# Optimization experiments

Measured on AMD Instinct MI355X. Metric: run time of the kernel, lower is better.

The kernel has to match this reference:

```python
import jax, jax.numpy as jnp
import numpy as np

B, S, D, H, NL, FE = 2, 1024, 1024, 16, 6, 4
HD = D // H
DFF = D * FE
EPS = 1e-5


def setup_inputs() -> dict:
    key = jax.random.key(0)
    ks = jax.random.split(key, 12)
    sd = 0.02
    n = lambda k, sh: (jax.random.normal(k, sh, jnp.float32) * sd)
    return {
        "x": jax.random.normal(ks[0], (B, S, D), jnp.float32),
        "pos": n(ks[1], (1, S, D)),
        "Wq": n(ks[2], (NL, HD, HD)), "bq": jnp.zeros((NL, HD), jnp.float32),
        "Wk": n(ks[3], (NL, HD, HD)), "bk": jnp.zeros((NL, HD), jnp.float32),
        "Wv": n(ks[4], (NL, HD, HD)), "bv": jnp.zeros((NL, HD), jnp.float32),
        "Wfc": n(ks[5], (NL, D, D)), "bfc": jnp.zeros((NL, D), jnp.float32),
        "ln1_w": jnp.ones((NL, D), jnp.float32), "ln1_b": jnp.zeros((NL, D), jnp.float32),
        "ln2_w": jnp.ones((NL, D), jnp.float32), "ln2_b": jnp.zeros((NL, D), jnp.float32),
        "W1": n(ks[6], (NL, D, DFF)), "b1": jnp.zeros((NL, DFF), jnp.float32),
        "W2": n(ks[7], (NL, DFF, D)), "b2": jnp.zeros((NL, D), jnp.float32),
        "lnf_w": jnp.ones((D,), jnp.float32), "lnf_b": jnp.zeros((D,), jnp.float32),
    }


def _ln(z, w, b):
    m = jnp.mean(z, axis=-1, keepdims=True)
    v = jnp.mean(jnp.square(z - m), axis=-1, keepdims=True)
    return (z - m) * jax.lax.rsqrt(v + EPS) * w + b


def reference(x, pos, Wq, bq, Wk, bk, Wv, bv, Wfc, bfc,
              ln1_w, ln1_b, ln2_w, ln2_b, W1, b1, W2, b2, lnf_w, lnf_b):
    Bx, Sx, Dx = x.shape
    causal = jnp.tril(jnp.ones((Sx, Sx), bool))  # [S,S], broadcast over b,h
    y = x + pos[:, :Sx, :]
    scale = 1.0 / jnp.sqrt(jnp.float32(HD))
    for i in range(NL):
        yh = y.reshape(Bx, Sx, H, HD)
        # per-head Linear with weights SHARED across heads (as in source)
        q = yh @ Wq[i] + bq[i]
        k = yh @ Wk[i] + bk[i]
        v = yh @ Wv[i] + bv[i]
        score = jnp.einsum("bqhd,bkhd->bhqk", q, k)
        # masked_fill(-1e20) BEFORE scaling, as in source
        score = jnp.where(causal, score, jnp.float32(-1e20)) * scale
        attn = jax.nn.softmax(score, axis=-1)
        o = jnp.einsum("bhqk,bkhd->bqhd", attn, v).reshape(Bx, Sx, D)
        o = o @ Wfc[i] + bfc[i]
        add = _ln(o + y, ln1_w[i], ln1_b[i])
        ff = jax.nn.gelu(add @ W1[i] + b1[i], approximate=False) @ W2[i] + b2[i]
        y = _ln(ff + add, ln2_w[i], ln2_b[i])
    return _ln(y, lnf_w, lnf_b)
```

## Files before the change

kernel.cpp:

```cpp
#include <hip/hip_runtime.h>
#include <hip/hip_bf16.h>
#include <math.h>

#define B_   2
#define S_   1024
#define D_   1024
#define H_   16
#define HD_  64
#define NL_  6
#define DFF_ 4096

typedef __bf16 bf16_t;
typedef bf16_t bf16x8 __attribute__((ext_vector_type(8)));
typedef bf16_t bf16x4 __attribute__((ext_vector_type(4)));
typedef float  f32x4  __attribute__((ext_vector_type(4)));

__device__ __forceinline__ float gelu_exact(float x) {
    return 0.5f * x * (1.0f + erff(x * 0.70710678118654752f));
}

__device__ __forceinline__ void gload16(const bf16_t* g, bf16_t* l) {
    __builtin_amdgcn_global_load_lds(
        (const __attribute__((address_space(1))) void*)g,
        (__attribute__((address_space(3))) void*)l, 16, 0, 0);
}

__global__ __launch_bounds__(256) void add_pos_kernel(
    const float* __restrict__ x, const float* __restrict__ pos,
    float* __restrict__ y, bf16_t* __restrict__ yb)
{
    int idx = blockIdx.x * 256 + threadIdx.x;
    f32x4 xv = *(const f32x4*)&x[idx * 4];
    f32x4 pv = *(const f32x4*)&pos[(idx & 262143) * 4];
    f32x4 o = xv + pv;
    *(f32x4*)&y[idx * 4] = o;
    *(bf16x4*)&yb[idx * 4] = __builtin_convertvector(o, bf16x4);
}

__global__ __launch_bounds__(256) void qkv_mfma_kernel(
    const bf16_t* __restrict__ yb,
    const float* __restrict__ Wq, const float* __restrict__ bq,
    const float* __restrict__ Wk, const float* __restrict__ bk,
    const float* __restrict__ Wv, const float* __restrict__ bv,
    bf16_t* __restrict__ q, bf16_t* __restrict__ k, bf16_t* __restrict__ v)
{
    __shared__ __align__(16) bf16_t As[128][72];
    __shared__ __align__(16) bf16_t Wt[3][64][72];

    int tid = threadIdx.x;
    long m0 = (long)blockIdx.x * 128;

#pragma unroll
    for (int it = 0; it < 4; ++it) {
        int c = it * 256 + tid;
        int row = c >> 3, col = (c & 7) * 8;
        *(bf16x8*)&As[row][col] = *(const bf16x8*)&yb[(m0 + row) * 64 + col];
    }
#pragma unroll
    for (int it = 0; it < 16; ++it) {
        int i = it * 256 + tid;
        int r = i >> 6, c = i & 63;
        Wt[0][c][r] = (bf16_t)Wq[i];
        Wt[1][c][r] = (bf16_t)Wk[i];
        Wt[2][c][r] = (bf16_t)Wv[i];
    }
    __syncthreads();

    int wave = tid >> 6, lane = tid & 63;
    int quad = lane >> 4, l16 = lane & 15;
    int wm = wave * 32;

    bf16x8 a[2][2];
#pragma unroll
    for (int i = 0; i < 2; ++i)
#pragma unroll
        for (int ks = 0; ks < 2; ++ks)
            a[i][ks] = *(bf16x8*)&As[wm + i * 16 + l16][ks * 32 + quad * 8];

    f32x4 acc[3][2][4];
#pragma unroll
    for (int o = 0; o < 3; ++o)
#pragma unroll
        for (int i = 0; i < 2; ++i)
#pragma unroll
            for (int j = 0; j < 4; ++j) acc[o][i][j] = (f32x4)0.f;

#pragma unroll
    for (int o = 0; o < 3; ++o)
#pragma unroll
        for (int j = 0; j < 4; ++j) {
            bf16x8 b0 = *(bf16x8*)&Wt[o][j * 16 + l16][quad * 8];
            bf16x8 b1 = *(bf16x8*)&Wt[o][j * 16 + l16][32 + quad * 8];
#pragma unroll
            for (int i = 0; i < 2; ++i) {
                acc[o][i][j] = __builtin_amdgcn_mfma_f32_16x16x32_bf16(a[i][0], b0, acc[o][i][j], 0, 0, 0);
                acc[o][i][j] = __builtin_amdgcn_mfma_f32_16x16x32_bf16(a[i][1], b1, acc[o][i][j], 0, 0, 0);
            }
        }

    bf16_t* outs[3] = { q, k, v };
    const float* biases[3] = { bq, bk, bv };
#pragma unroll
    for (int o = 0; o < 3; ++o)
#pragma unroll
        for (int j = 0; j < 4; ++j) {
            int col = j * 16 + l16;
            float bias = biases[o][col];
#pragma unroll
            for (int i = 0; i < 2; ++i) {
                long rbase = m0 + wm + i * 16 + quad * 4;
#pragma unroll
                for (int r = 0; r < 4; ++r)
                    outs[o][(rbase + r) * 64 + col] = (bf16_t)(acc[o][i][j][r] + bias);
            }
        }
}

__global__ __launch_bounds__(256) void vtrans_kernel(
    const bf16_t* __restrict__ vb, bf16_t* __restrict__ vT)
{
    __shared__ __align__(16) bf16_t L[32][72];
    int tid = threadIdx.x;
    int s0 = blockIdx.x * 32;
    int bh = blockIdx.y;
    int b = bh >> 4, h = bh & 15;
    int sr = tid >> 3, dc = (tid & 7) * 8;
    *(bf16x8*)&L[sr][dc] =
        *(const bf16x8*)&vb[(((long)b * S_ + s0 + sr) * H_ + h) * HD_ + dc];
    __syncthreads();
    int dr = tid >> 2, sg = (tid & 3) * 8;
    bf16x8 o;
#pragma unroll
    for (int j = 0; j < 8; ++j) o[j] = L[sg + j][dr];
    *(bf16x8*)&vT[((long)bh * HD_ + dr) * S_ + s0 + sg] = o;
}

__global__ __launch_bounds__(256) void attn_mfma_kernel(
    const bf16_t* __restrict__ Q, const bf16_t* __restrict__ K,
    const bf16_t* __restrict__ VT, bf16_t* __restrict__ Ob)
{
    __shared__ __align__(16) bf16_t Ks[32][72];
    __shared__ __align__(16) bf16_t Vt[64][40];
    __shared__ __align__(16) bf16_t Ps[4][16][40];

    int tid = threadIdx.x;
    int wave = tid >> 6, lane = tid & 63;
    int quad = lane >> 4, l16 = lane & 15;
    int q0 = blockIdx.x * 64;
    int bh = blockIdx.y;
    int b = bh >> 4, h = bh & 15;
    int qw = q0 + wave * 16;
    const float scale = 0.125f;
    const float MASKED = -1.25e19f;

    const bf16_t* Qbase = Q + (((long)b * S_ + qw + l16) * H_ + h) * HD_;
    bf16x8 aq0 = *(const bf16x8*)&Qbase[quad * 8];
    bf16x8 aq1 = *(const bf16x8*)&Qbase[32 + quad * 8];

    float mrun = -3.0e38f, lrun = 0.f;
    f32x4 oacc[4];
#pragma unroll
    for (int n = 0; n < 4; ++n) oacc[n] = (f32x4)0.f;

    int srow = tid >> 3, scol = (tid & 7) * 8;
    int vdr = tid >> 2, vkg = (tid & 3) * 8;
    const bf16_t* VTbase = VT + ((long)bh * HD_ + vdr) * S_ + vkg;
    int qg = qw + l16;

    int nkt = (q0 + 64) / 32;
    for (int kt = 0; kt < nkt; ++kt) {
        int k0 = kt * 32;
        __syncthreads();
        *(bf16x8*)&Ks[srow][scol] =
            *(const bf16x8*)&K[(((long)b * S_ + k0 + srow) * H_ + h) * HD_ + scol];
        *(bf16x8*)&Vt[vdr][vkg] = *(const bf16x8*)&VTbase[k0];
        __syncthreads();

        if (k0 > qw + 15) continue;

        f32x4 sc[2];
        sc[0] = (f32x4)0.f; sc[1] = (f32x4)0.f;
#pragma unroll
        for (int n = 0; n < 2; ++n) {
            bf16x8 ak0 = *(bf16x8*)&Ks[n * 16 + l16][quad * 8];
            bf16x8 ak1 = *(bf16x8*)&Ks[n * 16 + l16][32 + quad * 8];
            sc[n] = __builtin_amdgcn_mfma_f32_16x16x32_bf16(ak0, aq0, sc[n], 0, 0, 0);
            sc[n] = __builtin_amdgcn_mfma_f32_16x16x32_bf16(ak1, aq1, sc[n], 0, 0, 0);
        }
        float pmax = MASKED;
#pragma unroll
        for (int n = 0; n < 2; ++n)
#pragma unroll
            for (int r = 0; r < 4; ++r) {
                int kv = k0 + n * 16 + quad * 4 + r;
                float sv = (kv <= qg) ? sc[n][r] * scale : MASKED;
                sc[n][r] = sv;
                pmax = fmaxf(pmax, sv);
            }
        pmax = fmaxf(pmax, __shfl_xor(pmax, 16));
        pmax = fmaxf(pmax, __shfl_xor(pmax, 32));
        float mnew = fmaxf(mrun, pmax);
        float ls = 0.f;
#pragma unroll
        for (int n = 0; n < 2; ++n)
#pragma unroll
            for (int r = 0; r < 4; ++r) {
                float pv = __expf(sc[n][r] - mnew);
                sc[n][r] = pv;
                ls += pv;
            }
        ls += __shfl_xor(ls, 16);
        ls += __shfl_xor(ls, 32);
        float alpha = __expf(mrun - mnew);
        lrun = lrun * alpha + ls;
        mrun = mnew;

        *(bf16x4*)&Ps[wave][l16][quad * 4]      = __builtin_convertvector(sc[0], bf16x4);
        *(bf16x4*)&Ps[wave][l16][16 + quad * 4] = __builtin_convertvector(sc[1], bf16x4);

        f32x4 av;
#pragma unroll
        for (int r = 0; r < 4; ++r) av[r] = __shfl(alpha, quad * 4 + r);

        bf16x8 pa = *(bf16x8*)&Ps[wave][l16][quad * 8];
#pragma unroll
        for (int n = 0; n < 4; ++n) {
            bf16x8 bv = *(bf16x8*)&Vt[n * 16 + l16][quad * 8];
            oacc[n] = __builtin_amdgcn_mfma_f32_16x16x32_bf16(pa, bv, oacc[n] * av, 0, 0, 0);
        }
    }

    float inv = 1.0f / lrun;
    f32x4 iv;
#pragma unroll
    for (int r = 0; r < 4; ++r) iv[r] = __shfl(inv, quad * 4 + r);
#pragma unroll
    for (int r = 0; r < 4; ++r) {
        long rowbase = (((long)b * S_ + qw + quad * 4 + r) * H_ + h) * HD_;
#pragma unroll
        for (int n = 0; n < 4; ++n)
            Ob[rowbase + n * 16 + l16] = (bf16_t)(oacc[n][r] * iv[r]);
    }
}

__global__ void tconv_kernel(const float* __restrict__ W, bf16_t* __restrict__ Wt,
                             int Kd, int Nd)
{
    __shared__ float t[32][33];
    int tx = threadIdx.x, ty = threadIdx.y;
    int bx = blockIdx.x, by = blockIdx.y;
#pragma unroll
    for (int i = 0; i < 4; ++i)
        t[ty + i * 8][tx] = W[(size_t)(by * 32 + ty + i * 8) * Nd + bx * 32 + tx];
    __syncthreads();
#pragma unroll
    for (int i = 0; i < 4; ++i)
        Wt[(size_t)(bx * 32 + ty + i * 8) * Kd + by * 32 + tx] = (bf16_t)t[tx][ty + i * 8];
}

__global__ __launch_bounds__(256) void gemm_bt_kernel(
    const bf16_t* __restrict__ A, const bf16_t* __restrict__ Bt,
    const float* __restrict__ bias, float* __restrict__ Cf,
    bf16_t* __restrict__ Cb, int M, int N, int K, int act, size_t pstride)
{
    __shared__ __align__(16) bf16_t As[128 * 32];
    __shared__ __align__(16) bf16_t Bs[64 * 32];
    int tid = threadIdx.x;
    int wave = tid >> 6, lane = tid & 63;
    int quad = lane >> 4, l16 = lane & 15;
    int m0 = blockIdx.x * 128;
    int n0 = blockIdx.y * 64;
    int Kc = K / gridDim.z;
    int kbeg = blockIdx.z * Kc;
    int kend = kbeg + Kc;
    float* Cfp = Cf ? Cf + (size_t)blockIdx.z * pstride : nullptr;

    int wm = (wave >> 1) * 64, wn = (wave & 1) * 32;

    int srow = lane >> 2;
    int sslot = (lane & 3) ^ (srow & 3);
    int rslot = (quad ^ (l16 & 3)) * 8;

    f32x4 acc[4][2];
#pragma unroll
    for (int i = 0; i < 4; ++i)
#pragma unroll
        for (int j = 0; j < 2; ++j) acc[i][j] = (f32x4)0.f;

    const bf16_t* Ab = A + (size_t)(m0 + srow) * K + sslot * 8;
    const bf16_t* Bb = Bt + (size_t)(n0 + wave * 16 + srow) * K + sslot * 8;

    for (int k0 = kbeg; k0 < kend; k0 += 32) {
        __syncthreads();
#pragma unroll
        for (int t = 0; t < 2; ++t) {
            int seg = wave * 2 + t;
            gload16(Ab + (size_t)seg * 16 * K + k0, &As[seg * 512]);
        }
        gload16(Bb + k0, &Bs[wave * 512]);
        __syncthreads();

        bf16x8 af[4], bfr[2];
#pragma unroll
        for (int i = 0; i < 4; ++i)
            af[i] = *(bf16x8*)&As[(wm + i * 16 + l16) * 32 + rslot];
#pragma unroll
        for (int j = 0; j < 2; ++j)
            bfr[j] = *(bf16x8*)&Bs[(wn + j * 16 + l16) * 32 + rslot];
#pragma unroll
        for (int i = 0; i < 4; ++i)
#pragma unroll
            for (int j = 0; j < 2; ++j)
                acc[i][j] = __builtin_amdgcn_mfma_f32_16x16x32_bf16(
                    af[i], bfr[j], acc[i][j], 0, 0, 0);
    }

#pragma unroll
    for (int j = 0; j < 2; ++j) {
        int col = n0 + wn + j * 16 + l16;
        float bv = (bias && blockIdx.z == 0) ? bias[col] : 0.f;
#pragma unroll
        for (int i = 0; i < 4; ++i) {
            int rbase = m0 + wm + i * 16 + quad * 4;
#pragma unroll
            for (int r = 0; r < 4; ++r) {
                float vv = acc[i][j][r] + bv;
                if (act == 1) vv = gelu_exact(vv);
                if (Cfp) Cfp[(size_t)(rbase + r) * N + col] = vv;
                if (Cb) Cb[(size_t)(rbase + r) * N + col] = (bf16_t)vv;
            }
        }
    }
}

__global__ __launch_bounds__(256) void ln_fused_kernel(
    const float* __restrict__ a0, const float* __restrict__ a1,
    const float* __restrict__ b,
    const float* __restrict__ w, const float* __restrict__ beta,
    float* __restrict__ out, bf16_t* __restrict__ outb)
{
    long row = blockIdx.x;
    int tid = threadIdx.x;
    f32x4 z = *(const f32x4*)&a0[row * D_ + tid * 4];
    if (a1) z += *(const f32x4*)&a1[row * D_ + tid * 4];
    if (b)  z += *(const f32x4*)&b[row * D_ + tid * 4];
    float s  = z[0] + z[1] + z[2] + z[3];
    float ss = z[0]*z[0] + z[1]*z[1] + z[2]*z[2] + z[3]*z[3];
#pragma unroll
    for (int off = 32; off >= 1; off >>= 1) {
        s  += __shfl_down(s, off);
        ss += __shfl_down(ss, off);
    }
    __shared__ float red[8];
    int lane = tid & 63, wid = tid >> 6;
    if (lane == 0) { red[wid * 2] = s; red[wid * 2 + 1] = ss; }
    __syncthreads();
    s  = red[0] + red[2] + red[4] + red[6];
    ss = red[1] + red[3] + red[5] + red[7];
    float mean = s * (1.0f / D_);
    float var  = ss * (1.0f / D_) - mean * mean;
    float rs = rsqrtf(var + 1e-5f);
    f32x4 wv = *(const f32x4*)&w[tid * 4];
    f32x4 bv = *(const f32x4*)&beta[tid * 4];
    f32x4 o = (z - mean) * rs * wv + bv;
    *(f32x4*)&out[row * D_ + tid * 4] = o;
    if (outb) *(bf16x4*)&outb[row * D_ + tid * 4] = __builtin_convertvector(o, bf16x4);
}

extern "C" void kernel_launch(void* const* d_in, const int* in_sizes, int n_in,
                              void* d_out, int out_size, void* d_ws, size_t ws_size,
                              hipStream_t stream)
{
    (void)in_sizes; (void)n_in; (void)out_size; (void)ws_size;
    const float* x    = (const float*)d_in[0];
    const float* pos  = (const float*)d_in[1];
    const float* Wq   = (const float*)d_in[2];
    const float* bq   = (const float*)d_in[3];
    const float* Wk   = (const float*)d_in[4];
    const float* bk   = (const float*)d_in[5];
    const float* Wv   = (const float*)d_in[6];
    const float* bv   = (const float*)d_in[7];
    const float* Wfc  = (const float*)d_in[8];
    const float* bfc  = (const float*)d_in[9];
    const float* ln1w = (const float*)d_in[10];
    const float* ln1b = (const float*)d_in[11];
    const float* ln2w = (const float*)d_in[12];
    const float* ln2b = (const float*)d_in[13];
    const float* W1   = (const float*)d_in[14];
    const float* b1   = (const float*)d_in[15];
    const float* W2   = (const float*)d_in[16];
    const float* b2   = (const float*)d_in[17];
    const float* lnfw = (const float*)d_in[18];
    const float* lnfb = (const float*)d_in[19];

    const size_t MB = 1 << 20;
    char* ws = (char*)d_ws;
    float*  y    = (float*)(ws);
    bf16_t* yb   = (bf16_t*)(ws + 8 * MB);
    bf16_t* qb   = (bf16_t*)(ws + 12 * MB);
    bf16_t* kb   = (bf16_t*)(ws + 16 * MB);
    bf16_t* vb   = (bf16_t*)(ws + 20 * MB);
    bf16_t* ob   = (bf16_t*)(ws + 24 * MB);
    float*  t1a  = (float*)(ws + 12 * MB);
    float*  t1b  = (float*)(ws + 28 * MB);
    float*  t2a  = (float*)(ws + 12 * MB);
    float*  t2b  = (float*)(ws + 20 * MB);
    float*  add  = (float*)(ws + 28 * MB);
    bf16_t* addb = (bf16_t*)(ws + 36 * MB);
    bf16_t* vTb  = (bf16_t*)(ws + 40 * MB);
    bf16_t* ffb  = (bf16_t*)(ws + 40 * MB);
    bf16_t* WT   = (bf16_t*)(ws + 56 * MB);

    const size_t pstride_wfc  = (size_t)16 * MB / sizeof(float);
    const size_t pstride_ffn2 = (size_t)8 * MB / sizeof(float);

    add_pos_kernel<<<2048, 256, 0, stream>>>(x, pos, y, yb);

    for (int i = 0; i < NL_; ++i) {
        qkv_mfma_kernel<<<256, 256, 0, stream>>>(
            yb, Wq + i * 4096, bq + i * 64, Wk + i * 4096, bk + i * 64,
            Wv + i * 4096, bv + i * 64, qb, kb, vb);

        vtrans_kernel<<<dim3(32, 32), 256, 0, stream>>>(vb, vTb);

        attn_mfma_kernel<<<dim3(16, 32), 256, 0, stream>>>(qb, kb, vTb, ob);

        tconv_kernel<<<dim3(32, 32), dim3(32, 8), 0, stream>>>(
            Wfc + (size_t)i * D_ * D_, WT, D_, D_);
        gemm_bt_kernel<<<dim3(16, 16, 2), 256, 0, stream>>>(
            ob, WT, bfc + i * D_, t1a, nullptr, 2048, D_, D_, 0, pstride_wfc);

        ln_fused_kernel<<<2048, 256, 0, stream>>>(
            t1a, t1b, y, ln1w + i * D_, ln1b + i * D_, add, addb);

        tconv_kernel<<<dim3(128, 32), dim3(32, 8), 0, stream>>>(
            W1 + (size_t)i * D_ * DFF_, WT, D_, DFF_);
        gemm_bt_kernel<<<dim3(16, 64, 1), 256, 0, stream>>>(
            addb, WT, b1 + i * DFF_, nullptr, ffb, 2048, DFF_, D_, 1, 0);

        tconv_kernel<<<dim3(32, 128), dim3(32, 8), 0, stream>>>(
            W2 + (size_t)i * DFF_ * D_, WT, DFF_, D_);
        gemm_bt_kernel<<<dim3(16, 16, 2), 256, 0, stream>>>(
            ffb, WT, b2 + i * D_, t2a, nullptr, 2048, D_, DFF_, 0, pstride_ffn2);

        ln_fused_kernel<<<2048, 256, 0, stream>>>(
            t2a, t2b, add, ln2w + i * D_, ln2b + i * D_, y, yb);
    }

    ln_fused_kernel<<<2048, 256, 0, stream>>>(
        y, nullptr, nullptr, lnfw, lnfb, (float*)d_out, nullptr);
}
```

Before: 1.294 ms.

## Triple-buffer LDS in GEMM to overlap async global loads with MFMA

The bf16 GEMM kernel now keeps three LDS stages and prefetches tiles two K-steps ahead using global_load_lds. It waits on them with explicit vmcnt counters and a single barrier per iteration. The old loop used two barriers per K-step and stalled on each load before computing. The goal is to hide global memory latency behind the MFMA work. In exchange LDS use per block triples, which may lower occupancy, and the hand-coded waitcnt assumes exactly three loads per stage and at least two K-tiles.

Measured after the change: 1.242 ms. 4.0% less time.

```diff
diff --git a/kernel.cpp b/kernel.cpp
--- a/kernel.cpp
+++ b/kernel.cpp
@@ -263,8 +263,8 @@
     const float* __restrict__ bias, float* __restrict__ Cf,
     bf16_t* __restrict__ Cb, int M, int N, int K, int act, size_t pstride)
 {
-    __shared__ __align__(16) bf16_t As[128 * 32];
-    __shared__ __align__(16) bf16_t Bs[64 * 32];
+    __shared__ __align__(16) bf16_t As[3][128 * 32];
+    __shared__ __align__(16) bf16_t Bs[3][64 * 32];
     int tid = threadIdx.x;
     int wave = tid >> 6, lane = tid & 63;
     int quad = lane >> 4, l16 = lane & 15;
@@ -272,7 +272,6 @@
     int n0 = blockIdx.y * 64;
     int Kc = K / gridDim.z;
     int kbeg = blockIdx.z * Kc;
-    int kend = kbeg + Kc;
     float* Cfp = Cf ? Cf + (size_t)blockIdx.z * pstride : nullptr;
 
     int wm = (wave >> 1) * 64, wn = (wave & 1) * 32;
@@ -289,31 +288,52 @@
 
     const bf16_t* Ab = A + (size_t)(m0 + srow) * K + sslot * 8;
     const bf16_t* Bb = Bt + (size_t)(n0 + wave * 16 + srow) * K + sslot * 8;
-
-    for (int k0 = kbeg; k0 < kend; k0 += 32) {
-        __syncthreads();
-#pragma unroll
-        for (int t = 0; t < 2; ++t) {
-            int seg = wave * 2 + t;
-            gload16(Ab + (size_t)seg * 16 * K + k0, &As[seg * 512]);
-        }
-        gload16(Bb + k0, &Bs[wave * 512]);
-        __syncthreads();
-
-        bf16x8 af[4], bfr[2];
-#pragma unroll
-        for (int i = 0; i < 4; ++i)
-            af[i] = *(bf16x8*)&As[(wm + i * 16 + l16) * 32 + rslot];
-#pragma unroll
-        for (int j = 0; j < 2; ++j)
-            bfr[j] = *(bf16x8*)&Bs[(wn + j * 16 + l16) * 32 + rslot];
-#pragma unroll
-        for (int i = 0; i < 4; ++i)
-#pragma unroll
-            for (int j = 0; j < 2; ++j)
-                acc[i][j] = __builtin_amdgcn_mfma_f32_16x16x32_bf16(
-                    af[i], bfr[j], acc[i][j], 0, 0, 0);
-    }
+    int seg0 = wave * 2;
+    int nt = Kc >> 5;
+
+    #define STAGE(t, buf) do {                                                      \
+        int kk_ = kbeg + (t) * 32;                                                  \
+        gload16(Ab + (size_t)seg0 * 16 * K + kk_, &As[(buf)][seg0 * 512]);          \
+        gload16(Ab + (size_t)(seg0 + 1) * 16 * K + kk_, &As[(buf)][(seg0+1) * 512]);\
+        gload16(Bb + kk_, &Bs[(buf)][wave * 512]);                                  \
+    } while (0)
+
+    #define COMPUTE(buf) do {                                                       \
+        bf16x8 af[4], bfr[2];                                                       \
+        _Pragma("unroll")                                                           \
+        for (int i = 0; i < 4; ++i)                                                 \
+            af[i] = *(bf16x8*)&As[(buf)][(wm + i * 16 + l16) * 32 + rslot];         \
+        _Pragma("unroll")                                                           \
+        for (int j = 0; j < 2; ++j)                                                 \
+            bfr[j] = *(bf16x8*)&Bs[(buf)][(wn + j * 16 + l16) * 32 + rslot];        \
+        _Pragma("unroll")                                                           \
+        for (int i = 0; i < 4; ++i)                                                 \
+            _Pragma("unroll")                                                       \
+            for (int j = 0; j < 2; ++j)                                             \
+                acc[i][j] = __builtin_amdgcn_mfma_f32_16x16x32_bf16(                \
+                    af[i], bfr[j], acc[i][j], 0, 0, 0);                             \
+    } while (0)
+
+    STAGE(0, 0);
+    STAGE(1, 1);
+
+    int cur = 0, pf = 2;
+    for (int t = 0; t < nt - 1; ++t) {
+        asm volatile("s_waitcnt vmcnt(3)" ::: "memory");
+        __builtin_amdgcn_s_barrier();
+        __builtin_amdgcn_sched_barrier(0);
+        if (t + 2 < nt) STAGE(t + 2, pf);
+        COMPUTE(cur);
+        cur = (cur == 2) ? 0 : cur + 1;
+        pf  = (pf  == 2) ? 0 : pf  + 1;
+    }
+    asm volatile("s_waitcnt vmcnt(0)" ::: "memory");
+    __builtin_amdgcn_s_barrier();
+    __builtin_amdgcn_sched_barrier(0);
+    COMPUTE(cur);
+
+    #undef STAGE
+    #undef COMPUTE
 
 #pragma unroll
     for (int j = 0; j < 2; ++j) {
```
